# Kernel optimization log

Measured on AMD Instinct MI355X. Metric: run time of the kernel, lower is better.

The kernel has to match this reference:

```python
import jax, jax.numpy as jnp
import numpy as np

MARGIN = 0.1  # init kwarg


def setup_inputs() -> dict:
    key = jax.random.key(0)
    k1, k2, k3 = jax.random.split(key, 3)
    B, P, D = 256, 64, 1024
    imFtr = jax.random.normal(k1, (B, P, D), dtype=jnp.float32)
    disFtr = jax.random.normal(k2, (B, D), dtype=jnp.float32)
    lblList = jax.random.randint(k3, (B,), 0, 100000, dtype=jnp.int64 if jax.config.read('jax_enable_x64') else jnp.int32)
    return {"imFtr": imFtr, "disFtr": disFtr, "lblList": lblList}


def reference(imFtr, disFtr, lblList):
    B, P, D = imFtr.shape
    # simMM: [B*P, B] -> [B, P, B]; max over proposals P -> simMax [B, B]
    simMM = jnp.einsum('bpd,cd->bpc', imFtr, disFtr)
    simMax = jnp.max(simMM, axis=1)  # [B, B] (rows: image/video i, cols: text j)
    pos = jnp.diagonal(simMax)       # [B]

    # valid negative pairs: labels differ (diagonal excluded automatically)
    mask = (lblList[:, None] != lblList[None, :]).astype(simMax.dtype)  # [B, B]
    pairNum = jnp.sum(mask)

    # image -> text ranking: relu(sim[i, j] - sim[i, i] + margin)
    loss_it = jnp.sum(jnp.maximum(simMax - pos[:, None] + MARGIN, 0.0) * mask)
    loss = loss_it / pairNum

    # biLossFlag: text -> image ranking: relu(sim[j, i] - sim[i, i] + margin)
    loss_ti = jnp.sum(jnp.maximum(simMax - pos[None, :] + MARGIN, 0.0) * mask)
    loss = loss + jnp.where(pairNum > 0, loss_ti / pairNum, 0.0)

    return loss.reshape(1)
```

## Files before the change

kernel.cpp:

```cpp
#include <hip/hip_runtime.h>

constexpr int NB = 256;
constexpr int NP = 64;
constexpr int ND = 1024;
constexpr float MARGIN = 0.1f;

typedef __attribute__((ext_vector_type(8))) short short8;
typedef __attribute__((ext_vector_type(4))) float f32x4;

static __device__ inline unsigned short f2bf(float f) {
  unsigned u = __builtin_bit_cast(unsigned, f);
  u += 0x7fffu + ((u >> 16) & 1u);
  return (unsigned short)(u >> 16);
}

static __device__ inline short8 cvt8(float4 a, float4 b) {
  short8 r;
  r[0] = (short)f2bf(a.x); r[1] = (short)f2bf(a.y);
  r[2] = (short)f2bf(a.z); r[3] = (short)f2bf(a.w);
  r[4] = (short)f2bf(b.x); r[5] = (short)f2bf(b.y);
  r[6] = (short)f2bf(b.z); r[7] = (short)f2bf(b.w);
  return r;
}

__global__ __launch_bounds__(512) void simmax_kernel(
    const float* __restrict__ imFtr, const float* __restrict__ disFtr,
    float* __restrict__ simMax) {
  const int i  = blockIdx.x;
  const int t  = threadIdx.x;
  const int w  = t >> 6;
  const int l  = t & 63;
  const int lr = l & 15;
  const int lk = l >> 4;

  __shared__ short Asl[NP][64];

  f32x4 acc[4][2];
#pragma unroll
  for (int pt = 0; pt < 4; ++pt)
#pragma unroll
    for (int ct = 0; ct < 2; ++ct)
#pragma unroll
      for (int r = 0; r < 4; ++r) acc[pt][ct][r] = 0.0f;

  const int ar  = t >> 3;
  const int aks = t & 7;
  const float* ap = imFtr + (size_t)i * NP * ND + (size_t)ar * ND + aks * 8;
  const int wslot = ((aks ^ (ar & 7)) * 8);
  float4 av0 = *reinterpret_cast<const float4*>(ap);
  float4 av1 = *reinterpret_cast<const float4*>(ap + 4);

  const float* bp0 = disFtr + (size_t)(w * 32 + lr) * ND + lk * 8;
  const float* bp1 = disFtr + (size_t)(w * 32 + 16 + lr) * ND + lk * 8;

  for (int kc = 0; kc < 16; ++kc) {
    const int kbase = kc * 64;
    float4 bld[2][2][2];
#pragma unroll
    for (int ks = 0; ks < 2; ++ks) {
      const int ko = kbase + ks * 32;
      bld[ks][0][0] = *reinterpret_cast<const float4*>(bp0 + ko);
      bld[ks][0][1] = *reinterpret_cast<const float4*>(bp0 + ko + 4);
      bld[ks][1][0] = *reinterpret_cast<const float4*>(bp1 + ko);
      bld[ks][1][1] = *reinterpret_cast<const float4*>(bp1 + ko + 4);
    }
    __syncthreads();
    *reinterpret_cast<short8*>(&Asl[ar][wslot]) = cvt8(av0, av1);
    if (kc < 15) {
      const float* apn = ap + (kc + 1) * 64;
      av0 = *reinterpret_cast<const float4*>(apn);
      av1 = *reinterpret_cast<const float4*>(apn + 4);
    }
    __syncthreads();

#pragma unroll
    for (int ks = 0; ks < 2; ++ks) {
      short8 bfr0 = cvt8(bld[ks][0][0], bld[ks][0][1]);
      short8 bfr1 = cvt8(bld[ks][1][0], bld[ks][1][1]);
#pragma unroll
      for (int pt = 0; pt < 4; ++pt) {
        const int row  = pt * 16 + lr;
        const int slot = (((ks * 4 + lk) ^ (row & 7)) * 8);
        short8 afr = *reinterpret_cast<const short8*>(&Asl[row][slot]);
        acc[pt][0] = __builtin_amdgcn_mfma_f32_16x16x32_bf16(afr, bfr0, acc[pt][0], 0, 0, 0);
        acc[pt][1] = __builtin_amdgcn_mfma_f32_16x16x32_bf16(afr, bfr1, acc[pt][1], 0, 0, 0);
      }
    }
  }

#pragma unroll
  for (int ct = 0; ct < 2; ++ct) {
    float m = acc[0][ct][0];
#pragma unroll
    for (int pt = 0; pt < 4; ++pt)
#pragma unroll
      for (int r = 0; r < 4; ++r) m = fmaxf(m, acc[pt][ct][r]);
    m = fmaxf(m, __shfl_xor(m, 16));
    m = fmaxf(m, __shfl_xor(m, 32));
    if (l < 16) simMax[(size_t)i * NB + w * 32 + ct * 16 + l] = m;
  }
}

__global__ __launch_bounds__(256) void loss_kernel(
    const float* __restrict__ simMax, const int* __restrict__ lbl,
    float* __restrict__ partial) {
  const int i = blockIdx.x;
  const int j = threadIdx.x;
  __shared__ float posi_sh;
  __shared__ float red[3][4];

  float s = simMax[(size_t)i * NB + j];
  if (j == i) posi_sh = s;
  __syncthreads();
  const float posi = posi_sh;
  const float posj = simMax[(size_t)j * NB + j];

  const float msk = (lbl[i] != lbl[j]) ? 1.0f : 0.0f;
  float c  = msk;
  float l1 = msk * fmaxf(s - posi + MARGIN, 0.0f);
  float l2 = msk * fmaxf(s - posj + MARGIN, 0.0f);
#pragma unroll
  for (int o = 32; o > 0; o >>= 1) {
    c  += __shfl_down(c, o);
    l1 += __shfl_down(l1, o);
    l2 += __shfl_down(l2, o);
  }
  const int w = j >> 6;
  if ((j & 63) == 0) { red[0][w] = c; red[1][w] = l1; red[2][w] = l2; }
  __syncthreads();
  if (j == 0) {
    partial[i * 3 + 0] = red[0][0] + red[0][1] + red[0][2] + red[0][3];
    partial[i * 3 + 1] = red[1][0] + red[1][1] + red[1][2] + red[1][3];
    partial[i * 3 + 2] = red[2][0] + red[2][1] + red[2][2] + red[2][3];
  }
}

__global__ __launch_bounds__(256) void finalize_kernel(
    const float* __restrict__ partial, float* __restrict__ out) {
  const int t = threadIdx.x;
  __shared__ float red[3][4];
  float c  = partial[t * 3 + 0];
  float l1 = partial[t * 3 + 1];
  float l2 = partial[t * 3 + 2];
#pragma unroll
  for (int o = 32; o > 0; o >>= 1) {
    c  += __shfl_down(c, o);
    l1 += __shfl_down(l1, o);
    l2 += __shfl_down(l2, o);
  }
  const int w = t >> 6;
  if ((t & 63) == 0) { red[0][w] = c; red[1][w] = l1; red[2][w] = l2; }
  __syncthreads();
  if (t == 0) {
    float cs  = red[0][0] + red[0][1] + red[0][2] + red[0][3];
    float l1s = red[1][0] + red[1][1] + red[1][2] + red[1][3];
    float l2s = red[2][0] + red[2][1] + red[2][2] + red[2][3];
    float loss = l1s / cs;
    loss += (cs > 0.0f) ? (l2s / cs) : 0.0f;
    out[0] = loss;
  }
}

extern "C" void kernel_launch(void* const* d_in, const int* in_sizes, int n_in,
                              void* d_out, int out_size, void* d_ws, size_t ws_size,
                              hipStream_t stream) {
  (void)in_sizes; (void)n_in; (void)out_size; (void)ws_size;
  const float* imFtr  = (const float*)d_in[0];
  const float* disFtr = (const float*)d_in[1];
  const int*   lbl    = (const int*)d_in[2];
  float* out = (float*)d_out;

  float* simMax  = (float*)d_ws;
  float* partial = (float*)((char*)d_ws + (size_t)NB * NB * 4);

  simmax_kernel<<<dim3(NB), dim3(512), 0, stream>>>(imFtr, disFtr, simMax);
  loss_kernel<<<dim3(NB), dim3(256), 0, stream>>>(simMax, lbl, partial);
  finalize_kernel<<<dim3(1), dim3(256), 0, stream>>>(partial, out);
}
```

Baseline: 41.10 us.

## Pre-convert disFtr to bf16, split proposals across two blocks, double-buffer A tiles

Adds a small kernel that converts disFtr to bf16 once, so each simmax block stops re-converting B from fp32 on every pass. The main kernel now splits the 64 proposals into two halves across blockIdx.y, doubling the grid to 512 blocks, and uses a double-buffered LDS A tile with 128-wide K chunks and register-prefetched B. The loss kernel takes the max of the two half results. The cost is an extra launch and workspace; a fallback path keeps the old kernel when the workspace is too small.

Result: slower. 46.71 us (+13.6%).

```diff
diff --git a/kernel.cpp b/kernel.cpp
--- a/kernel.cpp
+++ b/kernel.cpp
@@ -5,7 +5,8 @@
 constexpr int ND = 1024;
 constexpr float MARGIN = 0.1f;
 
-typedef __attribute__((ext_vector_type(8))) short short8;
+typedef __attribute__((ext_vector_type(8))) short bf16x8;
+typedef __attribute__((ext_vector_type(4))) short bf16x4;
 typedef __attribute__((ext_vector_type(4))) float f32x4;
 
 static __device__ inline unsigned short f2bf(float f) {
@@ -14,8 +15,8 @@
   return (unsigned short)(u >> 16);
 }
 
-static __device__ inline short8 cvt8(float4 a, float4 b) {
-  short8 r;
+static __device__ inline bf16x8 cvt8(float4 a, float4 b) {
+  bf16x8 r;
   r[0] = (short)f2bf(a.x); r[1] = (short)f2bf(a.y);
   r[2] = (short)f2bf(a.z); r[3] = (short)f2bf(a.w);
   r[4] = (short)f2bf(b.x); r[5] = (short)f2bf(b.y);
@@ -23,7 +24,112 @@
   return r;
 }
 
-__global__ __launch_bounds__(512) void simmax_kernel(
+__global__ __launch_bounds__(256) void cvtB_kernel(
+    const float* __restrict__ src, short* __restrict__ dst) {
+  const int idx = (blockIdx.x * 256 + threadIdx.x) * 4;
+  float4 v = *reinterpret_cast<const float4*>(src + idx);
+  bf16x4 r;
+  r[0] = (short)f2bf(v.x); r[1] = (short)f2bf(v.y);
+  r[2] = (short)f2bf(v.z); r[3] = (short)f2bf(v.w);
+  *reinterpret_cast<bf16x4*>(dst + idx) = r;
+}
+
+__global__ __launch_bounds__(512) void simmax_half_kernel(
+    const float* __restrict__ imFtr, const short* __restrict__ disB,
+    float* __restrict__ simHalf) {
+  const int i  = blockIdx.x;
+  const int ph = blockIdx.y;
+  const int t  = threadIdx.x;
+  const int w  = t >> 6;
+  const int l  = t & 63;
+  const int lr = l & 15;
+  const int lk = l >> 4;
+
+  __shared__ short Asl[2][32][128];
+
+  f32x4 acc[2][2];
+#pragma unroll
+  for (int pt = 0; pt < 2; ++pt)
+#pragma unroll
+    for (int ct = 0; ct < 2; ++ct)
+#pragma unroll
+      for (int r = 0; r < 4; ++r) acc[pt][ct][r] = 0.0f;
+
+  const int ar  = t >> 4;
+  const int aks = t & 15;
+  const float* ap = imFtr + ((size_t)i * NP + ph * 32 + ar) * ND + aks * 8;
+  short* awp0 = &Asl[0][ar][(aks ^ (ar & 7)) * 8];
+  short* awp1 = &Asl[1][ar][(aks ^ (ar & 7)) * 8];
+
+  const short* bp0 = disB + (size_t)(w * 32 + lr) * ND + lk * 8;
+  const short* bp1 = disB + (size_t)(w * 32 + 16 + lr) * ND + lk * 8;
+
+  float4 a0 = *reinterpret_cast<const float4*>(ap);
+  float4 a1 = *reinterpret_cast<const float4*>(ap + 4);
+  bf16x8 breg[4][2];
+#pragma unroll
+  for (int ks = 0; ks < 4; ++ks) {
+    breg[ks][0] = *reinterpret_cast<const bf16x8*>(bp0 + ks * 32);
+    breg[ks][1] = *reinterpret_cast<const bf16x8*>(bp1 + ks * 32);
+  }
+  *reinterpret_cast<bf16x8*>(awp0) = cvt8(a0, a1);
+  __syncthreads();
+
+#pragma unroll
+  for (int kc = 0; kc < 8; ++kc) {
+    float4 an0, an1;
+    bf16x8 bnext[4][2];
+    if (kc < 7) {
+      const float* apn = ap + (kc + 1) * 128;
+      an0 = *reinterpret_cast<const float4*>(apn);
+      an1 = *reinterpret_cast<const float4*>(apn + 4);
+      const int kb = (kc + 1) * 128;
+#pragma unroll
+      for (int ks = 0; ks < 4; ++ks) {
+        bnext[ks][0] = *reinterpret_cast<const bf16x8*>(bp0 + kb + ks * 32);
+        bnext[ks][1] = *reinterpret_cast<const bf16x8*>(bp1 + kb + ks * 32);
+      }
+    }
+    const int cb = kc & 1;
+#pragma unroll
+    for (int ks = 0; ks < 4; ++ks) {
+#pragma unroll
+      for (int pt = 0; pt < 2; ++pt) {
+        const int row  = pt * 16 + lr;
+        const int slot = ((ks * 4 + lk) ^ (row & 7)) * 8;
+        bf16x8 afr = *reinterpret_cast<const bf16x8*>(&Asl[cb][row][slot]);
+        acc[pt][0] = __builtin_amdgcn_mfma_f32_16x16x32_bf16(afr, breg[ks][0], acc[pt][0], 0, 0, 0);
+        acc[pt][1] = __builtin_amdgcn_mfma_f32_16x16x32_bf16(afr, breg[ks][1], acc[pt][1], 0, 0, 0);
+      }
+    }
+    if (kc < 7) {
+      bf16x8 aw = cvt8(an0, an1);
+      if ((kc & 1) == 0) *reinterpret_cast<bf16x8*>(awp1) = aw;
+      else               *reinterpret_cast<bf16x8*>(awp0) = aw;
+      __syncthreads();
+#pragma unroll
+      for (int ks = 0; ks < 4; ++ks) {
+        breg[ks][0] = bnext[ks][0];
+        breg[ks][1] = bnext[ks][1];
+      }
+    }
+  }
+
+#pragma unroll
+  for (int ct = 0; ct < 2; ++ct) {
+    float m = acc[0][ct][0];
+#pragma unroll
+    for (int pt = 0; pt < 2; ++pt)
+#pragma unroll
+      for (int r = 0; r < 4; ++r) m = fmaxf(m, acc[pt][ct][r]);
+    m = fmaxf(m, __shfl_xor(m, 16));
+    m = fmaxf(m, __shfl_xor(m, 32));
+    if (l < 16)
+      simHalf[((size_t)ph * NB + i) * NB + w * 32 + ct * 16 + l] = m;
+  }
+}
+
+__global__ __launch_bounds__(512) void simmax_fallback_kernel(
     const float* __restrict__ imFtr, const float* __restrict__ disFtr,
     float* __restrict__ simMax) {
   const int i  = blockIdx.x;
@@ -65,7 +171,7 @@
       bld[ks][1][1] = *reinterpret_cast<const float4*>(bp1 + ko + 4);
     }
     __syncthreads();
-    *reinterpret_cast<short8*>(&Asl[ar][wslot]) = cvt8(av0, av1);
+    *reinterpret_cast<bf16x8*>(&Asl[ar][wslot]) = cvt8(av0, av1);
     if (kc < 15) {
       const float* apn = ap + (kc + 1) * 64;
       av0 = *reinterpret_cast<const float4*>(apn);
@@ -75,13 +181,13 @@
 
 #pragma unroll
     for (int ks = 0; ks < 2; ++ks) {
-      short8 bfr0 = cvt8(bld[ks][0][0], bld[ks][0][1]);
-      short8 bfr1 = cvt8(bld[ks][1][0], bld[ks][1][1]);
+      bf16x8 bfr0 = cvt8(bld[ks][0][0], bld[ks][0][1]);
+      bf16x8 bfr1 = cvt8(bld[ks][1][0], bld[ks][1][1]);
 #pragma unroll
       for (int pt = 0; pt < 4; ++pt) {
         const int row  = pt * 16 + lr;
         const int slot = (((ks * 4 + lk) ^ (row & 7)) * 8);
-        short8 afr = *reinterpret_cast<const short8*>(&Asl[row][slot]);
+        bf16x8 afr = *reinterpret_cast<const bf16x8*>(&Asl[row][slot]);
         acc[pt][0] = __builtin_amdgcn_mfma_f32_16x16x32_bf16(afr, bfr0, acc[pt][0], 0, 0, 0);
         acc[pt][1] = __builtin_amdgcn_mfma_f32_16x16x32_bf16(afr, bfr1, acc[pt][1], 0, 0, 0);
       }
@@ -102,18 +208,18 @@
 }
 
 __global__ __launch_bounds__(256) void loss_kernel(
-    const float* __restrict__ simMax, const int* __restrict__ lbl,
-    float* __restrict__ partial) {
+    const float* __restrict__ sh0, const float* __restrict__ sh1,
+    const int* __restrict__ lbl, float* __restrict__ partial) {
   const int i = blockIdx.x;
   const int j = threadIdx.x;
   __shared__ float posi_sh;
   __shared__ float red[3][4];
 
-  float s = simMax[(size_t)i * NB + j];
+  float s = fmaxf(sh0[(size_t)i * NB + j], sh1[(size_t)i * NB + j]);
   if (j == i) posi_sh = s;
   __syncthreads();
   const float posi = posi_sh;
-  const float posj = simMax[(size_t)j * NB + j];
+  const float posj = fmaxf(sh0[(size_t)j * NB + j], sh1[(size_t)j * NB + j]);
 
   const float msk = (lbl[i] != lbl[j]) ? 1.0f : 0.0f;
   float c  = msk;
@@ -164,16 +270,31 @@
 extern "C" void kernel_launch(void* const* d_in, const int* in_sizes, int n_in,
                               void* d_out, int out_size, void* d_ws, size_t ws_size,
                               hipStream_t stream) {
-  (void)in_sizes; (void)n_in; (void)out_size; (void)ws_size;
+  (void)in_sizes; (void)n_in; (void)out_size;
   const float* imFtr  = (const float*)d_in[0];
   const float* disFtr = (const float*)d_in[1];
   const int*   lbl    = (const int*)d_in[2];
   float* out = (float*)d_out;
 
-  float* simMax  = (float*)d_ws;
-  float* partial = (float*)((char*)d_ws + (size_t)NB * NB * 4);
-
-  simmax_kernel<<<dim3(NB), dim3(512), 0, stream>>>(imFtr, disFtr, simMax);
-  loss_kernel<<<dim3(NB), dim3(256), 0, stream>>>(simMax, lbl, partial);
-  finalize_kernel<<<dim3(1), dim3(256), 0, stream>>>(partial, out);
-}
+  const size_t disB_bytes = (size_t)NB * ND * sizeof(short);
+  const size_t half_bytes = (size_t)NB * NB * sizeof(float);
+  const size_t need = disB_bytes + 2 * half_bytes + 3 * NB * sizeof(float);
+
+  if (ws_size >= need) {
+    short* disB    = (short*)d_ws;
+    float* simHalf = (float*)((char*)d_ws + disB_bytes);
+    float* partial = (float*)((char*)d_ws + disB_bytes + 2 * half_bytes);
+
+    cvtB_kernel<<<dim3(NB), dim3(256), 0, stream>>>(disFtr, disB);
+    simmax_half_kernel<<<dim3(NB, 2), dim3(512), 0, stream>>>(imFtr, disB, simHalf);
+    loss_kernel<<<dim3(NB), dim3(256), 0, stream>>>(simHalf, simHalf + (size_t)NB * NB,
+                                                    lbl, partial);
+    finalize_kernel<<<dim3(1), dim3(256), 0, stream>>>(partial, out);
+  } else {
+    float* simMax  = (float*)d_ws;
+    float* partial = (float*)((char*)d_ws + (size_t)NB * NB * 4);
+    simmax_fallback_kernel<<<dim3(NB), dim3(512), 0, stream>>>(imFtr, disFtr, simMax);
+    loss_kernel<<<dim3(NB), dim3(256), 0, stream>>>(simMax, simMax, lbl, partial);
+    finalize_kernel<<<dim3(1), dim3(256), 0, stream>>>(partial, out);
+  }
+}
```
